# Kernel optimization log

Hardware: AMD Instinct MI355X
Metric: run time of the kernel (lower is better)

Reference implementation:

```python
import jax, jax.numpy as jnp
import numpy as np

N = 100000   # n_nodes (= ninput, identity features)
E = 1600000  # edges per adjacency (avg degree 16)
H = 128      # nhid
EPS = 1e-12


def setup_inputs() -> dict:
    key = jax.random.key(0)
    ks = jax.random.split(key, 24)
    inp = {
        'adj1_rows': jax.random.randint(ks[0], (E,), 0, N),
        'adj1_cols': jax.random.randint(ks[1], (E,), 0, N),
        'adj1_vals': jax.random.uniform(ks[2], (E,), jnp.float32) / 16.0,
        'adj2_rows': jax.random.randint(ks[3], (E,), 0, N),
        'adj2_cols': jax.random.randint(ks[4], (E,), 0, N),
        'adj2_vals': jax.random.uniform(ks[5], (E,), jnp.float32) / 16.0,
    }
    s = 1.0 / np.sqrt(H)
    inp['w1'] = jax.random.uniform(ks[6], (N, H), jnp.float32, -s, s)
    for i in range(2, 10):
        inp[f'w{i}'] = jax.random.uniform(ks[5 + i], (H, H), jnp.float32, -s, s)
    s2 = 1.0 / np.sqrt(2 * H)
    inp['m1'] = jax.random.uniform(ks[15], (H, 2 * H), jnp.float32, -s, s)
    inp['b1'] = jnp.zeros((2 * H,), jnp.float32)
    inp['m2'] = jax.random.uniform(ks[16], (2 * H, 2 * H), jnp.float32, -s2, s2)
    inp['b2'] = jnp.zeros((2 * H,), jnp.float32)
    inp['m3'] = jax.random.uniform(ks[17], (2 * H, 1), jnp.float32, -s2, s2)
    inp['b3'] = jnp.zeros((1,), jnp.float32)
    return inp


def _spmm(rows, cols, vals, x):
    # sparse [N,N] @ dense [N,H] via gather + segment_sum
    return jax.ops.segment_sum(vals[:, None] * x[cols], rows, num_segments=N)


def _l2norm(x):
    # F.normalize(x, p=2, dim=1)
    n = jnp.sqrt(jnp.sum(x * x, axis=1, keepdims=True))
    return x / jnp.maximum(n, EPS)


def _mlp(x, m1, b1, m2, b2, m3, b3):
    # dropout inactive (eval mode) for deterministic reference
    h = jax.nn.relu(x @ m1 + b1)
    h = jax.nn.relu(h @ m2 + b2)
    return h @ m3 + b3  # [N,1]


def _branch(rows, cols, vals, w1, ws, mlp_params):
    x = jax.nn.relu(_spmm(rows, cols, vals, w1))
    x = _l2norm(x)
    score = _mlp(x, *mlp_params)
    for i, w in enumerate(ws):
        x = jax.nn.relu(_spmm(rows, cols, vals, x @ w))
        if i < len(ws) - 1:  # last layer (gc9) is relu only, no normalize
            x = _l2norm(x)
        score = score + _mlp(x, *mlp_params)
    return score


def reference(adj1_rows, adj1_cols, adj1_vals, adj2_rows, adj2_cols, adj2_vals,
              w1, w2, w3, w4, w5, w6, w7, w8, w9,
              m1, b1, m2, b2, m3, b3):
    ws = [w2, w3, w4, w5, w6, w7, w8, w9]
    mlp_params = (m1, b1, m2, b2, m3, b3)
    score1 = _branch(adj1_rows, adj1_cols, adj1_vals, w1, ws, mlp_params)
    score2 = _branch(adj2_rows, adj2_cols, adj2_vals, w1, ws, mlp_params)
    return score1 * score2  # [N,1]
```

## Files before the change

kernel.cpp:

```cpp
#include <hip/hip_runtime.h>
#include <hip/hip_fp16.h>

#define NN 100000
#define NE 1600000
#define HD 128
#define HD2 256

#define NBK 512
#define RPB 196
#define CH  4096
#define CAP 4096

typedef unsigned int u32;
typedef unsigned short u16;
typedef _Float16 half8 __attribute__((ext_vector_type(8)));
typedef float floatx4 __attribute__((ext_vector_type(4)));

static inline int cdiv(int a, int b){ return (a + b - 1) / b; }

__device__ __forceinline__ u32 split_pack(float v){
  __half h;
  if(fabsf(v) < 6.103515625e-05f) h = __ushort_as_half((u16)0);
  else h = __float2half_rn(v);
  float hf = __half2float(h);
  __half l = __float2half_rn((v - hf) * 4096.0f);
  return (u32)__half_as_ushort(h) | ((u32)__half_as_ushort(l) << 16);
}

__global__ void k_setup(const float* __restrict__ w0, const float* __restrict__ w1,
                        const float* __restrict__ w2, const float* __restrict__ w3,
                        const float* __restrict__ w4, const float* __restrict__ w5,
                        const float* __restrict__ w6, const float* __restrict__ w7,
                        const float* __restrict__ m1, const float* __restrict__ m2,
                        u32* __restrict__ wbase, float* __restrict__ sc,
                        int* __restrict__ bcur){
  int bid = blockIdx.x;
  if(bid < 896){
    int idx = bid * 256 + threadIdx.x;
    const float* W; int K, N, local;
    if(idx < 131072){
      int wi = idx >> 14; local = idx & 16383; K = HD; N = HD;
      W = wi == 0 ? w0 : wi == 1 ? w1 : wi == 2 ? w2 : wi == 3 ? w3 :
          wi == 4 ? w4 : wi == 5 ? w5 : wi == 6 ? w6 : w7;
    } else if(idx < 163840){
      local = idx - 131072; K = HD; N = HD2; W = m1;
    } else {
      local = idx - 163840; K = HD2; N = HD2; W = m2;
    }
    int n = local / K, k = local - n * K;
    wbase[idx] = split_pack(W[(size_t)k * N + n]);
  } else if(bid < 896 + 782){
    int i = (bid - 896) * 256 + threadIdx.x;
    if(i < 2 * NN) sc[i] = 0.f;
  } else {
    int i = (bid - 896 - 782) * 256 + threadIdx.x;
    if(i < 2 * NBK) bcur[i] = (i & (NBK - 1)) * CAP;
  }
}

__global__ void k_binscatter(const int* __restrict__ r0a, const int* __restrict__ c0a,
                             const float* __restrict__ v0a,
                             const int* __restrict__ r1a, const int* __restrict__ c1a,
                             const float* __restrict__ v1a,
                             int* __restrict__ bcur,
                             u32* __restrict__ sr0, uint2* __restrict__ sv0,
                             u32* __restrict__ sr1, uint2* __restrict__ sv1){
  __shared__ int cnt[NBK];
  __shared__ int bstart[NBK];
  __shared__ int gbase[NBK];
  __shared__ int sh[256];
  __shared__ u32 srow[CH];
  __shared__ uint2 scvs[CH];
  int z = blockIdx.y;
  const int* rows = z ? r1a : r0a;
  const int* cols = z ? c1a : c0a;
  const float* vals = z ? v1a : v0a;
  int* cur = bcur + z * NBK;
  u32* osr = z ? sr1 : sr0;
  uint2* osv = z ? sv1 : sv0;
  int t = threadIdx.x;
  for(int i = t; i < NBK; i += 256) cnt[i] = 0;
  __syncthreads();
  int e0 = blockIdx.x * CH;
  int total = NE - e0; if(total > CH) total = CH;
  int r_[16], c_[16], b_[16], k_[16]; float v_[16];
  #pragma unroll
  for(int k = 0; k < 16; k++){
    int e = e0 + t + k * 256;
    b_[k] = -1;
    if(e < NE){
      r_[k] = rows[e]; c_[k] = cols[e]; v_[k] = vals[e];
      b_[k] = r_[k] / RPB;
      k_[k] = atomicAdd(&cnt[b_[k]], 1);
    }
  }
  __syncthreads();
  int v0 = cnt[2 * t], v1 = cnt[2 * t + 1];
  int s2 = v0 + v1;
  sh[t] = s2;
  __syncthreads();
  for(int d = 1; d < 256; d <<= 1){
    int tv = (t >= d) ? sh[t - d] : 0;
    __syncthreads();
    sh[t] += tv;
    __syncthreads();
  }
  int excl = sh[t] - s2;
  bstart[2 * t] = excl;
  bstart[2 * t + 1] = excl + v0;
  __syncthreads();
  #pragma unroll
  for(int k = 0; k < 16; k++){
    if(b_[k] >= 0){
      int slot = bstart[b_[k]] + k_[k];
      srow[slot] = (u32)r_[k];
      scvs[slot] = make_uint2((u32)c_[k], __float_as_uint(v_[k]));
    }
  }
  for(int b = t; b < NBK; b += 256){
    int c = cnt[b];
    if(c > 0) gbase[b] = atomicAdd(&cur[b], c);
  }
  __syncthreads();
  for(int i = t; i < total; i += 256){
    u32 r = srow[i];
    int b = (int)r / RPB;
    int dest = gbase[b] + (i - bstart[b]);
    osr[dest] = r;
    osv[dest] = scvs[i];
  }
}

__global__ void k_bucket_scan(const int* __restrict__ bcur, int* __restrict__ bbase,
                              int* __restrict__ c1ptr, int* __restrict__ c2ptr){
  __shared__ int sh[256];
  int z = blockIdx.x;
  const int* cur = bcur + z * NBK;
  int* bb = bbase + z * NBK;
  int t = threadIdx.x;
  int v0 = cur[2 * t]     - (2 * t) * CAP;
  int v1 = cur[2 * t + 1] - (2 * t + 1) * CAP;
  int s2 = v0 + v1;
  sh[t] = s2;
  __syncthreads();
  for(int d = 1; d < 256; d <<= 1){
    int tv = (t >= d) ? sh[t - d] : 0;
    __syncthreads();
    sh[t] += tv;
    __syncthreads();
  }
  int excl = sh[t] - s2;
  bb[2 * t] = excl;
  bb[2 * t + 1] = excl + v0;
  if(t == 0){
    int* rp = z ? c2ptr : c1ptr;
    rp[NN] = NE;
  }
}

__global__ void k_bucket_place(const int* __restrict__ bcur, const int* __restrict__ bbase,
                               const u32* __restrict__ sr0, const uint2* __restrict__ sv0,
                               const u32* __restrict__ sr1, const uint2* __restrict__ sv1,
                               int* __restrict__ c1ptr, int* __restrict__ c2ptr,
                               uint2* __restrict__ e0, uint2* __restrict__ e1){
  __shared__ int hist[RPB];
  __shared__ int cur[RPB];
  __shared__ int sh[256];
  __shared__ u32 srows[CAP];
  int z = blockIdx.y;
  int b = blockIdx.x;
  int r0 = b * RPB;
  if(r0 >= NN) return;
  int rend = r0 + RPB; if(rend > NN) rend = NN;
  int nr = rend - r0;
  const u32* sr = z ? sr1 : sr0;
  const uint2* sv = z ? sv1 : sv0;
  int* rp = z ? c2ptr : c1ptr;
  uint2* ecv = z ? e1 : e0;
  int cnt = bcur[z * NBK + b] - b * CAP;
  int base = bbase[z * NBK + b];
  int g = b * CAP;
  int t = threadIdx.x;
  for(int r = t; r < nr; r += 256) hist[r] = 0;
  __syncthreads();
  for(int i = t; i < cnt; i += 256){
    u32 r = sr[g + i];
    srows[i] = r;
    atomicAdd(&hist[(int)r - r0], 1);
  }
  __syncthreads();
  int v = (t < nr) ? hist[t] : 0;
  sh[t] = v;
  __syncthreads();
  for(int d = 1; d < 256; d <<= 1){
    int tv = (t >= d) ? sh[t - d] : 0;
    __syncthreads();
    sh[t] += tv;
    __syncthreads();
  }
  int excl = sh[t] - v;
  if(t < nr){
    rp[r0 + t] = base + excl;
    cur[t] = base + excl;
  }
  __syncthreads();
  for(int i = t; i < cnt; i += 256){
    int r = (int)srows[i] - r0;
    int p = atomicAdd(&cur[r], 1);
    ecv[p] = sv[g + i];
  }
}

template<bool NORM>
__global__ void k_spmm(const int* __restrict__ rowptr, const uint2* __restrict__ ecv,
                       const float* __restrict__ X, u32* __restrict__ outpk){
  int node = (blockIdx.x << 2) + (threadIdx.x >> 6);
  int lane = threadIdx.x & 63;
  if(node >= NN) return;
  int h = lane >> 5, s = lane & 31;
  int sb = rowptr[node], e = rowptr[node + 1];
  float ax = 0.f, ay = 0.f, az = 0.f, aw = 0.f;
  int i = sb;
  for(; i + 15 < e; i += 16){
    uint2 ee[8]; float4 xx[8];
    #pragma unroll
    for(int j = 0; j < 8; j++) ee[j] = ecv[i + 2 * j + h];
    #pragma unroll
    for(int j = 0; j < 8; j++) xx[j] = *(const float4*)(X + (size_t)ee[j].x * HD + s * 4);
    #pragma unroll
    for(int j = 0; j < 8; j++){
      float vv = __uint_as_float(ee[j].y);
      ax = fmaf(vv, xx[j].x, ax);
      ay = fmaf(vv, xx[j].y, ay);
      az = fmaf(vv, xx[j].z, az);
      aw = fmaf(vv, xx[j].w, aw);
    }
  }
  for(; i + 7 < e; i += 8){
    uint2 ee[4]; float4 xx[4];
    #pragma unroll
    for(int j = 0; j < 4; j++) ee[j] = ecv[i + 2 * j + h];
    #pragma unroll
    for(int j = 0; j < 4; j++) xx[j] = *(const float4*)(X + (size_t)ee[j].x * HD + s * 4);
    #pragma unroll
    for(int j = 0; j < 4; j++){
      float vv = __uint_as_float(ee[j].y);
      ax = fmaf(vv, xx[j].x, ax);
      ay = fmaf(vv, xx[j].y, ay);
      az = fmaf(vv, xx[j].z, az);
      aw = fmaf(vv, xx[j].w, aw);
    }
  }
  for(; i < e; i += 2){
    int idx = i + h;
    bool ok = idx < e;
    uint2 f = ecv[ok ? idx : i];
    float vv = ok ? __uint_as_float(f.y) : 0.f;
    float4 xv = *(const float4*)(X + (size_t)f.x * HD + s * 4);
    ax = fmaf(vv, xv.x, ax);
    ay = fmaf(vv, xv.y, ay);
    az = fmaf(vv, xv.z, az);
    aw = fmaf(vv, xv.w, aw);
  }
  ax += __shfl_xor(ax, 32, 64);
  ay += __shfl_xor(ay, 32, 64);
  az += __shfl_xor(az, 32, 64);
  aw += __shfl_xor(aw, 32, 64);
  ax = fmaxf(ax, 0.f); ay = fmaxf(ay, 0.f);
  az = fmaxf(az, 0.f); aw = fmaxf(aw, 0.f);
  if(NORM){
    float ss = ax * ax + ay * ay + az * az + aw * aw;
    #pragma unroll
    for(int o = 16; o >= 1; o >>= 1) ss += __shfl_xor(ss, o, 64);
    float scale = 1.f / fmaxf(sqrtf(ss), 1e-12f);
    ax *= scale; ay *= scale; az *= scale; aw *= scale;
  }
  if(h == 0){
    uint4 p;
    p.x = split_pack(ax); p.y = split_pack(ay);
    p.z = split_pack(az); p.w = split_pack(aw);
    *(uint4*)(outpk + (size_t)node * HD + s * 4) = p;
  }
}

template<int MODE>
__launch_bounds__(256, 2)
__global__ void k_mfma_gemm(const u32* __restrict__ Apk, const u32* __restrict__ Btpk,
                            const u32* __restrict__ Bt1pk,
                            const float* __restrict__ bias, float* __restrict__ Yout,
                            u32* __restrict__ Hout, const float* __restrict__ m3,
                            float* __restrict__ score, int M, int K, int N){
  __shared__ u16 As_h[128 * 40], As_l[128 * 40];
  __shared__ u16 Bs_h[128 * 40], Bs_l[128 * 40];
  constexpr int NYC = (MODE == 0) ? 1 : ((MODE == 3) ? 3 : 2);
  const int d = blockIdx.x;
  const int grp = d / (8 * NYC);
  const int rem = d - grp * 8 * NYC;
  const int rt = grp * 8 + (rem & 7);
  const int ct = rem >> 3;
  const int nrt = (M + 127) >> 7;
  if(rt >= nrt) return;
  const int tid = threadIdx.x;
  const int lane = tid & 63, wid = tid >> 6;
  const int lm = lane & 15, lg = lane >> 4;
  const int mq = (wid & 1) * 64, nq = (wid >> 1) * 64;
  const int m0 = rt * 128;
  int n0 = ct * 128;
  const u32* Bt = Btpk;
  bool m0path = true;
  if(MODE == 3){
    m0path = (ct == 0);
    if(m0path){ n0 = 0; }
    else      { n0 = (ct - 1) * 128; Bt = Bt1pk; }
  }

  floatx4 accA[4][4], accB[4][4];
  #pragma unroll
  for(int i = 0; i < 4; i++)
    #pragma unroll
    for(int j = 0; j < 4; j++){
      accA[i][j] = (floatx4){0.f, 0.f, 0.f, 0.f};
      accB[i][j] = (floatx4){0.f, 0.f, 0.f, 0.f};
    }

  for(int k0 = 0; k0 < K; k0 += 32){
    uint4 av[4], bv[4];
    #pragma unroll
    for(int j = 0; j < 4; j++){
      int li = tid + j * 256;
      int row = li >> 3, kc = (li & 7) * 4;
      int ar = m0 + row; if(ar >= M) ar = M - 1;
      av[j] = *(const uint4*)(Apk + (size_t)ar * K + k0 + kc);
      bv[j] = *(const uint4*)(Bt + (size_t)(n0 + row) * K + k0 + kc);
    }
    if(k0) __syncthreads();
    #pragma unroll
    for(int j = 0; j < 4; j++){
      int li = tid + j * 256;
      int row = li >> 3, kc = (li & 7) * 4;
      int base = row * 40 + kc;
      ushort4 h, l;
      h.x = (u16)(av[j].x & 0xffff); l.x = (u16)(av[j].x >> 16);
      h.y = (u16)(av[j].y & 0xffff); l.y = (u16)(av[j].y >> 16);
      h.z = (u16)(av[j].z & 0xffff); l.z = (u16)(av[j].z >> 16);
      h.w = (u16)(av[j].w & 0xffff); l.w = (u16)(av[j].w >> 16);
      *(ushort4*)&As_h[base] = h;
      *(ushort4*)&As_l[base] = l;
      h.x = (u16)(bv[j].x & 0xffff); l.x = (u16)(bv[j].x >> 16);
      h.y = (u16)(bv[j].y & 0xffff); l.y = (u16)(bv[j].y >> 16);
      h.z = (u16)(bv[j].z & 0xffff); l.z = (u16)(bv[j].z >> 16);
      h.w = (u16)(bv[j].w & 0xffff); l.w = (u16)(bv[j].w >> 16);
      *(ushort4*)&Bs_h[base] = h;
      *(ushort4*)&Bs_l[base] = l;
    }
    __syncthreads();

    half8 fa_h[4], fa_l[4], fb_h[4], fb_l[4];
    #pragma unroll
    for(int s = 0; s < 4; s++){
      int ra = (mq + s * 16 + lm) * 40 + lg * 8;
      fa_h[s] = *(const half8*)&As_h[ra];
      fa_l[s] = *(const half8*)&As_l[ra];
      int rb = (nq + s * 16 + lm) * 40 + lg * 8;
      fb_h[s] = *(const half8*)&Bs_h[rb];
      fb_l[s] = *(const half8*)&Bs_l[rb];
    }
    #pragma unroll
    for(int i = 0; i < 4; i++)
      #pragma unroll
      for(int j = 0; j < 4; j++){
        accA[i][j] = __builtin_amdgcn_mfma_f32_16x16x32_f16(fa_h[i], fb_h[j], accA[i][j], 0, 0, 0);
        accB[i][j] = __builtin_amdgcn_mfma_f32_16x16x32_f16(fa_h[i], fb_l[j], accB[i][j], 0, 0, 0);
        accB[i][j] = __builtin_amdgcn_mfma_f32_16x16x32_f16(fa_l[i], fb_h[j], accB[i][j], 0, 0, 0);
      }
  }

  const float inv4096 = 1.f / 4096.f;
  if(MODE == 0 || (MODE == 3 && m0path)){
    int ldy = (MODE == 3) ? HD : N;
    #pragma unroll
    for(int i = 0; i < 4; i++)
      #pragma unroll
      for(int r = 0; r < 4; r++){
        int m = m0 + mq + i * 16 + lg * 4 + r;
        if(m < M){
          #pragma unroll
          for(int j = 0; j < 4; j++){
            int c = n0 + nq + j * 16 + lm;
            Yout[(size_t)m * ldy + c] = accA[i][j][r] + accB[i][j][r] * inv4096;
          }
        }
      }
  } else if(MODE == 1 || MODE == 3){
    int ldh = (MODE == 3) ? HD2 : N;
    #pragma unroll
    for(int i = 0; i < 4; i++)
      #pragma unroll
      for(int r = 0; r < 4; r++){
        int m = m0 + mq + i * 16 + lg * 4 + r;
        if(m < M){
          #pragma unroll
          for(int j = 0; j < 4; j++){
            int c = n0 + nq + j * 16 + lm;
            float v = fmaxf(accA[i][j][r] + accB[i][j][r] * inv4096 + bias[c], 0.f);
            Hout[(size_t)m * ldh + c] = split_pack(v);
          }
        }
      }
  } else {
    #pragma unroll
    for(int i = 0; i < 4; i++)
      #pragma unroll
      for(int r = 0; r < 4; r++){
        float s = 0.f;
        #pragma unroll
        for(int j = 0; j < 4; j++){
          int c = n0 + nq + j * 16 + lm;
          float v = fmaxf(accA[i][j][r] + accB[i][j][r] * inv4096 + bias[c], 0.f);
          s = fmaf(v, m3[c], s);
        }
        s += __shfl_xor(s, 1, 64);
        s += __shfl_xor(s, 2, 64);
        s += __shfl_xor(s, 4, 64);
        s += __shfl_xor(s, 8, 64);
        int m = m0 + mq + i * 16 + lg * 4 + r;
        if(lm == 0 && m < M) atomicAdd(&score[m], s);
      }
  }
}

__global__ void k_final(const float* __restrict__ sc, const float* __restrict__ b3,
                        float* __restrict__ out){
  int i = blockIdx.x * 256 + threadIdx.x;
  if(i < NN){
    float b = 9.f * b3[0];
    out[i] = (sc[i] + b) * (sc[NN + i] + b);
  }
}

extern "C" void kernel_launch(void* const* d_in, const int* in_sizes, int n_in,
                              void* d_out, int out_size, void* d_ws, size_t ws_size,
                              hipStream_t stream){
  const int*   a1r = (const int*)d_in[0];
  const int*   a1c = (const int*)d_in[1];
  const float* a1v = (const float*)d_in[2];
  const int*   a2r = (const int*)d_in[3];
  const int*   a2c = (const int*)d_in[4];
  const float* a2v = (const float*)d_in[5];
  const float* w1  = (const float*)d_in[6];
  const float* w[8];
  for(int i = 0; i < 8; i++) w[i] = (const float*)d_in[7 + i];
  const float* m1 = (const float*)d_in[15];
  const float* b1 = (const float*)d_in[16];
  const float* m2 = (const float*)d_in[17];
  const float* b2 = (const float*)d_in[18];
  const float* m3 = (const float*)d_in[19];
  const float* b3 = (const float*)d_in[20];
  float* out = (float*)d_out;

  char* base = (char*)d_ws;
  size_t off = 0;
  auto alloc = [&](size_t bytes) -> char* {
    char* r = base + off;
    off += (bytes + 255) & ~(size_t)255;
    return r;
  };
  int*   c1ptr = (int*)  alloc((size_t)(NN + 1) * 4);
  int*   c2ptr = (int*)  alloc((size_t)(NN + 1) * 4);
  uint2* ecv1  = (uint2*)alloc((size_t)NE * 8);
  uint2* ecv2  = (uint2*)alloc((size_t)NE * 8);
  int*   cursor= (int*)  alloc((size_t)2 * NBK * 4);
  int*   bbase = (int*)  alloc((size_t)2 * NBK * 4);
  float* sc    = (float*)alloc((size_t)2 * NN * 4);
  u32*   wtpk[8];
  for(int i = 0; i < 8; i++) wtpk[i] = (u32*)alloc((size_t)HD * HD * 4);
  u32*   m1tpk = (u32*)alloc((size_t)HD2 * HD * 4);
  u32*   m2tpk = (u32*)alloc((size_t)HD2 * HD2 * 4);
  u32*   xpk   = (u32*)alloc((size_t)NN * HD * 4);
  u32*   h1pk  = (u32*)alloc((size_t)NN * HD2 * 4);
  size_t need_ded = off + (((size_t)NN * HD * 4 + 255) & ~(size_t)255);
  bool ded_y = (ws_size >= need_ded);
  float* y = ded_y ? (float*)alloc((size_t)NN * HD * 4) : (float*)h1pk;

  const size_t SZ = (size_t)NBK * CAP;
  char* hb = (char*)h1pk;
  uint2* sv1 = (uint2*)hb;
  u32*   sr1 = (u32*)(hb + SZ * 8);
  uint2* sv2 = (uint2*)(hb + SZ * 12);
  u32*   sr2 = (u32*)(hb + SZ * 20);

  hipLaunchKernelGGL(k_setup, dim3(896 + 782 + 4), dim3(256), 0, stream,
                     w[0], w[1], w[2], w[3], w[4], w[5], w[6], w[7], m1, m2,
                     wtpk[0], sc, cursor);
  hipLaunchKernelGGL(k_binscatter, dim3(cdiv(NE, CH), 2), dim3(256), 0, stream,
                     a1r, a1c, a1v, a2r, a2c, a2v, cursor, sr1, sv1, sr2, sv2);
  hipLaunchKernelGGL(k_bucket_scan, dim3(2), dim3(256), 0, stream, cursor, bbase, c1ptr, c2ptr);
  hipLaunchKernelGGL(k_bucket_place, dim3(NBK, 2), dim3(256), 0, stream,
                     cursor, bbase, sr1, sv1, sr2, sv2, c1ptr, c2ptr, ecv1, ecv2);

  const int NRT = cdiv(NN, 128);
  const int GP  = cdiv(NRT, 8) * 8;
  const int SPB = cdiv(NN, 4);
  auto mode1 = [&](){
    hipLaunchKernelGGL((k_mfma_gemm<1>), dim3(GP * 2), dim3(256), 0, stream,
                       xpk, m1tpk, (const u32*)nullptr, b1, (float*)nullptr, h1pk,
                       (const float*)nullptr, (float*)nullptr, NN, HD, HD2);
  };
  auto mode2 = [&](float* score){
    hipLaunchKernelGGL((k_mfma_gemm<2>), dim3(GP * 2), dim3(256), 0, stream,
                       h1pk, m2tpk, (const u32*)nullptr, b2, (float*)nullptr, (u32*)nullptr,
                       m3, score, NN, HD2, HD2);
  };
  auto gemm0 = [&](int i){
    hipLaunchKernelGGL((k_mfma_gemm<0>), dim3(GP * 1), dim3(256), 0, stream,
                       xpk, wtpk[i], (const u32*)nullptr, (const float*)nullptr, y, (u32*)nullptr,
                       (const float*)nullptr, (float*)nullptr, NN, HD, HD);
  };
  auto fused01 = [&](int i){
    hipLaunchKernelGGL((k_mfma_gemm<3>), dim3(GP * 3), dim3(256), 0, stream,
                       xpk, wtpk[i], m1tpk, b1, y, h1pk,
                       (const float*)nullptr, (float*)nullptr, NN, HD, 0);
  };

  for(int b = 0; b < 2; b++){
    const int* rp = b ? c2ptr : c1ptr;
    const uint2* ecv = b ? ecv2 : ecv1;
    float* score = sc + (size_t)b * NN;
    hipLaunchKernelGGL((k_spmm<true>), dim3(SPB), dim3(256), 0, stream,
                       rp, ecv, w1, xpk);
    if(ded_y){
      for(int i = 0; i < 8; i++){
        fused01(i);
        mode2(score);
        if(i < 7)
          hipLaunchKernelGGL((k_spmm<true>),  dim3(SPB), dim3(256), 0, stream,
                             rp, ecv, y, xpk);
        else
          hipLaunchKernelGGL((k_spmm<false>), dim3(SPB), dim3(256), 0, stream,
                             rp, ecv, y, xpk);
      }
      mode1();
      mode2(score);
    } else {
      mode1();
      mode2(score);
      for(int i = 0; i < 8; i++){
        gemm0(i);
        if(i < 7)
          hipLaunchKernelGGL((k_spmm<true>),  dim3(SPB), dim3(256), 0, stream,
                             rp, ecv, y, xpk);
        else
          hipLaunchKernelGGL((k_spmm<false>), dim3(SPB), dim3(256), 0, stream,
                             rp, ecv, y, xpk);
        mode1();
        mode2(score);
      }
    }
  }

  hipLaunchKernelGGL(k_final, dim3(cdiv(NN, 256)), dim3(256), 0, stream, sc, b3, out);
}
```

Before: 4.203 ms.

## Fuse layer GEMM with previous layer's MLP second stage via double-buffered hidden

Adds a dual-role GEMM kernel whose blocks run either the fused W/M1 GEMM for the current layer or the M2+score GEMM for the previous layer's hidden buffer. The hidden activations are double-buffered so the two can run in one launch. This cuts kernel launches and lets the two independent GEMMs fill the GPU together, reducing tail and launch gaps. The cost is an extra NN×256 workspace buffer, and the path runs only when the workspace is large enough.

```diff
diff --git a/kernel.cpp b/kernel.cpp
--- a/kernel.cpp
+++ b/kernel.cpp
@@ -284,16 +284,14 @@
 }
 
 template<int MODE>
-__launch_bounds__(256, 2)
-__global__ void k_mfma_gemm(const u32* __restrict__ Apk, const u32* __restrict__ Btpk,
+__device__ __forceinline__ void dev_gemm(int d,
+                            const u32* __restrict__ Apk, const u32* __restrict__ Btpk,
                             const u32* __restrict__ Bt1pk,
                             const float* __restrict__ bias, float* __restrict__ Yout,
                             u32* __restrict__ Hout, const float* __restrict__ m3,
-                            float* __restrict__ score, int M, int K, int N){
-  __shared__ u16 As_h[128 * 40], As_l[128 * 40];
-  __shared__ u16 Bs_h[128 * 40], Bs_l[128 * 40];
+                            float* __restrict__ score, int M, int K, int N,
+                            u16* As_h, u16* As_l, u16* Bs_h, u16* Bs_l){
   constexpr int NYC = (MODE == 0) ? 1 : ((MODE == 3) ? 3 : 2);
-  const int d = blockIdx.x;
   const int grp = d / (8 * NYC);
   const int rem = d - grp * 8 * NYC;
   const int rt = grp * 8 + (rem & 7);
@@ -427,6 +425,40 @@
         if(lm == 0 && m < M) atomicAdd(&score[m], s);
       }
   }
+}
+
+template<int MODE>
+__launch_bounds__(256, 2)
+__global__ void k_mfma_gemm(const u32* __restrict__ Apk, const u32* __restrict__ Btpk,
+                            const u32* __restrict__ Bt1pk,
+                            const float* __restrict__ bias, float* __restrict__ Yout,
+                            u32* __restrict__ Hout, const float* __restrict__ m3,
+                            float* __restrict__ score, int M, int K, int N){
+  __shared__ u16 As_h[128 * 40], As_l[128 * 40];
+  __shared__ u16 Bs_h[128 * 40], Bs_l[128 * 40];
+  dev_gemm<MODE>(blockIdx.x, Apk, Btpk, Bt1pk, bias, Yout, Hout, m3, score,
+                 M, K, N, As_h, As_l, Bs_h, Bs_l);
+}
+
+template<int MA, int MB>
+__launch_bounds__(256, 2)
+__global__ void k_dual(const u32* __restrict__ Aa, const u32* __restrict__ Ba,
+                       const u32* __restrict__ B1a, const float* __restrict__ biasa,
+                       float* __restrict__ Ya, u32* __restrict__ Ha,
+                       int Ma, int Ka, int Na,
+                       const u32* __restrict__ Ab, const u32* __restrict__ Bb,
+                       const float* __restrict__ biasb, const float* __restrict__ m3,
+                       float* __restrict__ score, int Mb, int Kb, int Nb, int GA){
+  __shared__ u16 As_h[128 * 40], As_l[128 * 40];
+  __shared__ u16 Bs_h[128 * 40], Bs_l[128 * 40];
+  if((int)blockIdx.x < GA)
+    dev_gemm<MA>(blockIdx.x, Aa, Ba, B1a, biasa, Ya, Ha,
+                 (const float*)nullptr, (float*)nullptr, Ma, Ka, Na,
+                 As_h, As_l, Bs_h, Bs_l);
+  else
+    dev_gemm<MB>((int)blockIdx.x - GA, Ab, Bb, (const u32*)nullptr, biasb,
+                 (float*)nullptr, (u32*)nullptr, m3, score, Mb, Kb, Nb,
+                 As_h, As_l, Bs_h, Bs_l);
 }
 
 __global__ void k_final(const float* __restrict__ sc, const float* __restrict__ b3,
@@ -481,6 +513,10 @@
   size_t need_ded = off + (((size_t)NN * HD * 4 + 255) & ~(size_t)255);
   bool ded_y = (ws_size >= need_ded);
   float* y = ded_y ? (float*)alloc((size_t)NN * HD * 4) : (float*)h1pk;
+  size_t need_ded2 = off + (((size_t)NN * HD2 * 4 + 255) & ~(size_t)255);
+  bool ded2 = ded_y && (ws_size >= need_ded2);
+  u32* h2pk = ded2 ? (u32*)alloc((size_t)NN * HD2 * 4) : h1pk;
+  u32* hbuf[2] = { h1pk, h2pk };
 
   const size_t SZ = (size_t)NBK * CAP;
   char* hb = (char*)h1pk;
@@ -501,14 +537,14 @@
   const int NRT = cdiv(NN, 128);
   const int GP  = cdiv(NRT, 8) * 8;
   const int SPB = cdiv(NN, 4);
-  auto mode1 = [&](){
+  auto mode1 = [&](u32* hdst){
     hipLaunchKernelGGL((k_mfma_gemm<1>), dim3(GP * 2), dim3(256), 0, stream,
-                       xpk, m1tpk, (const u32*)nullptr, b1, (float*)nullptr, h1pk,
+                       xpk, m1tpk, (const u32*)nullptr, b1, (float*)nullptr, hdst,
                        (const float*)nullptr, (float*)nullptr, NN, HD, HD2);
   };
-  auto mode2 = [&](float* score){
+  auto mode2 = [&](float* score, const u32* hsrc){
     hipLaunchKernelGGL((k_mfma_gemm<2>), dim3(GP * 2), dim3(256), 0, stream,
-                       h1pk, m2tpk, (const u32*)nullptr, b2, (float*)nullptr, (u32*)nullptr,
+                       hsrc, m2tpk, (const u32*)nullptr, b2, (float*)nullptr, (u32*)nullptr,
                        m3, score, NN, HD2, HD2);
   };
   auto gemm0 = [&](int i){
@@ -516,10 +552,20 @@
                        xpk, wtpk[i], (const u32*)nullptr, (const float*)nullptr, y, (u32*)nullptr,
                        (const float*)nullptr, (float*)nullptr, NN, HD, HD);
   };
-  auto fused01 = [&](int i){
+  auto fused01 = [&](int i, u32* hdst){
     hipLaunchKernelGGL((k_mfma_gemm<3>), dim3(GP * 3), dim3(256), 0, stream,
-                       xpk, wtpk[i], m1tpk, b1, y, h1pk,
+                       xpk, wtpk[i], m1tpk, b1, y, hdst,
                        (const float*)nullptr, (float*)nullptr, NN, HD, 0);
+  };
+  auto dual32 = [&](int i, u32* hdst, const u32* hsrc, float* score){
+    hipLaunchKernelGGL((k_dual<3, 2>), dim3(GP * 3 + GP * 2), dim3(256), 0, stream,
+                       xpk, wtpk[i], m1tpk, b1, y, hdst, NN, HD, 0,
+                       hsrc, m2tpk, b2, m3, score, NN, HD2, HD2, GP * 3);
+  };
+  auto dual12 = [&](u32* hdst, const u32* hsrc, float* score){
+    hipLaunchKernelGGL((k_dual<1, 2>), dim3(GP * 2 + GP * 2), dim3(256), 0, stream,
+                       xpk, m1tpk, (const u32*)nullptr, b1, (float*)nullptr, hdst, NN, HD, HD2,
+                       hsrc, m2tpk, b2, m3, score, NN, HD2, HD2, GP * 2);
   };
 
   for(int b = 0; b < 2; b++){
@@ -528,10 +574,12 @@
     float* score = sc + (size_t)b * NN;
     hipLaunchKernelGGL((k_spmm<true>), dim3(SPB), dim3(256), 0, stream,
                        rp, ecv, w1, xpk);
-    if(ded_y){
-      for(int i = 0; i < 8; i++){
-        fused01(i);
-        mode2(score);
+    if(ded2){
+      fused01(0, hbuf[0]);
+      hipLaunchKernelGGL((k_spmm<true>), dim3(SPB), dim3(256), 0, stream,
+                         rp, ecv, y, xpk);
+      for(int i = 1; i < 8; i++){
+        dual32(i, hbuf[i & 1], hbuf[(i - 1) & 1], score);
         if(i < 7)
           hipLaunchKernelGGL((k_spmm<true>),  dim3(SPB), dim3(256), 0, stream,
                              rp, ecv, y, xpk);
@@ -539,11 +587,24 @@
           hipLaunchKernelGGL((k_spmm<false>), dim3(SPB), dim3(256), 0, stream,
                              rp, ecv, y, xpk);
       }
-      mode1();
-      mode2(score);
+      dual12(hbuf[0], hbuf[1], score);
+      mode2(score, hbuf[0]);
+    } else if(ded_y){
+      for(int i = 0; i < 8; i++){
+        fused01(i, h1pk);
+        mode2(score, h1pk);
+        if(i < 7)
+          hipLaunchKernelGGL((k_spmm<true>),  dim3(SPB), dim3(256), 0, stream,
+                             rp, ecv, y, xpk);
+        else
+          hipLaunchKernelGGL((k_spmm<false>), dim3(SPB), dim3(256), 0, stream,
+                             rp, ecv, y, xpk);
+      }
+      mode1(h1pk);
+      mode2(score, h1pk);
     } else {
-      mode1();
-      mode2(score);
+      mode1(h1pk);
+      mode2(score, h1pk);
       for(int i = 0; i < 8; i++){
         gemm0(i);
         if(i < 7)
@@ -552,8 +613,8 @@
         else
           hipLaunchKernelGGL((k_spmm<false>), dim3(SPB), dim3(256), 0, stream,
                              rp, ecv, y, xpk);
-        mode1();
-        mode2(score);
+        mode1(h1pk);
+        mode2(score, h1pk);
       }
     }
   }
```

New measurement: 4.197 ms. Within noise of the previous version (-0.2%).
